# Kernel tuning notes

Measured on AMD Instinct MI355X. Metric: run time of the kernel, lower is better.

The kernel has to match this reference:

```python
import jax, jax.numpy as jnp
import numpy as np

N = 100000        # nodes
E = 1600000       # edges
D = 32            # hidden dim
C = 2             # num classes
NL = 4            # layer_num - 1 GIN layers
G = 512           # graphs in batch
BN_EPS = 1e-3     # keras BatchNormalization default epsilon


def setup_inputs() -> dict:
    key = jax.random.key(0)
    ks = jax.random.split(key, 16)
    s = 0.1
    return {
        "node_embeddings": jax.random.normal(ks[0], (N, D), dtype=jnp.float32),
        "edge_index": jax.random.randint(ks[1], (2, E), 0, N, dtype=jnp.int32),
        "batch": jnp.sort(jax.random.randint(ks[2], (N,), 0, G, dtype=jnp.int32)),
        # MLP inner dense + BN (per GIN layer)
        "W1": jax.random.normal(ks[3], (NL, D, D), dtype=jnp.float32) * s,
        "b1": jnp.zeros((NL, D), jnp.float32),
        "bn1_g": jnp.ones((NL, D), jnp.float32),
        "bn1_b": jnp.zeros((NL, D), jnp.float32),
        # MLP output dense
        "W2": jax.random.normal(ks[4], (NL, D, D), dtype=jnp.float32) * s,
        "b2": jnp.zeros((NL, D), jnp.float32),
        # ApplyNodeFunc BN
        "bn2_g": jnp.ones((NL, D), jnp.float32),
        "bn2_b": jnp.zeros((NL, D), jnp.float32),
        # outer per-layer BN
        "norm_g": jnp.ones((NL, D), jnp.float32),
        "norm_b": jnp.zeros((NL, D), jnp.float32),
        # readout heads: one Dense(num_classes) per hidden_rep level (layer_num of them)
        "dense_W": jax.random.normal(ks[5], (NL + 1, D, C), dtype=jnp.float32) * s,
        "dense_b": jnp.zeros((NL + 1, C), jnp.float32),
    }


def _bn(x, g, b):
    # inference-mode BatchNorm with init moving stats (mean=0, var=1)
    return x * (g / jnp.sqrt(1.0 + BN_EPS)) + b


def reference(node_embeddings, edge_index, batch, W1, b1, bn1_g, bn1_b,
              W2, b2, bn2_g, bn2_b, norm_g, norm_b, dense_W, dense_b):
    src, dst = edge_index[0], edge_index[1]
    h = node_embeddings
    hidden = [h]
    for i in range(NL):
        # GIN aggregation: (1+eps)*h + sum of neighbor features (eps=0)
        agg = jax.ops.segment_sum(h[src], dst, num_segments=N)  # [N, D]
        z = h + agg
        # ApplyNodeFunc: MLP (Dense->BN->ReLU->Dense) then BN + ReLU
        z = jax.nn.relu(_bn(z @ W1[i] + b1[i], bn1_g[i], bn1_b[i]))
        z = z @ W2[i] + b2[i]
        z = jax.nn.relu(_bn(z, bn2_g[i], bn2_b[i]))
        # outer norm + relu
        h = jax.nn.relu(_bn(z, norm_g[i], norm_b[i]))
        hidden.append(h)
    # readout: segment-sum pooling per hidden level, Dense(num_classes), summed
    score = jnp.zeros((G, C), dtype=node_embeddings.dtype)
    for i, hr in enumerate(hidden):
        pool = jax.ops.segment_sum(hr, batch, num_segments=G)  # [G, D]
        score = score + pool @ dense_W[i] + dense_b[i]
    return jax.nn.softmax(score, axis=-1)
```

## Files before the change

### kernel.cpp

```cpp
#include <hip/hip_runtime.h>
#include <hip/hip_fp16.h>

#define NN 100000
#define EE 1600000
#define DD 32
#define CC 2
#define NLAYERS 4
#define GG 512

#define BSH 9
#define BW 512
#define NBUK ((NN + BW - 1) / BW)
#define CAP 12288
#define CH 2048
#define NPART ((EE + CH - 1) / CH)

__global__ void part_kernel(const int* __restrict__ ei,
                            int* __restrict__ gcur,
                            unsigned* __restrict__ part) {
    __shared__ unsigned sorted[CH];
    __shared__ unsigned char sbkt[CH];
    __shared__ int cnt[NBUK], offs[NBUK], cur[NBUK], gbs[NBUK];

    const int tid = threadIdx.x;
    const int eb  = blockIdx.x * CH;
    const int nch = min(CH, EE - eb);

    for (int b = tid; b < NBUK; b += 256) cnt[b] = 0;
    __syncthreads();
    for (int i = tid; i < nch; i += 256) {
        int dn = ei[EE + eb + i];
        atomicAdd(&cnt[dn >> BSH], 1);
    }
    __syncthreads();
    if (tid == 0) {
        int o = 0;
        for (int b = 0; b < NBUK; ++b) { offs[b] = o; o += cnt[b]; }
    }
    __syncthreads();
    if (tid < NBUK) {
        cur[tid] = offs[tid];
        gbs[tid] = cnt[tid] ? atomicAdd(&gcur[tid], cnt[tid]) : 0;
    }
    __syncthreads();
    for (int i = tid; i < nch; i += 256) {
        int s  = ei[eb + i];
        int dn = ei[EE + eb + i];
        int b  = dn >> BSH;
        unsigned pk = ((unsigned)(dn & (BW - 1)) << 17) | (unsigned)s;
        int p = atomicAdd(&cur[b], 1);
        sorted[p] = pk;
        sbkt[p]   = (unsigned char)b;
    }
    __syncthreads();
    for (int i = tid; i < nch; i += 256) {
        int b = sbkt[i];
        part[(size_t)b * CAP + gbs[b] + (i - offs[b])] = sorted[i];
    }
}

__global__ void bscan_kernel(const int* __restrict__ gcur,
                             int* __restrict__ bbase,
                             int* __restrict__ row_ptr) {
    if (threadIdx.x == 0 && blockIdx.x == 0) {
        int o = 0;
        for (int b = 0; b < NBUK; ++b) { bbase[b] = o; o += gcur[b]; }
        row_ptr[NN] = EE;
    }
}

__global__ void lcsr_kernel(const unsigned* __restrict__ part,
                            const int* __restrict__ gcur,
                            const int* __restrict__ bbase,
                            int* __restrict__ row_ptr,
                            int* __restrict__ csr_src) {
    __shared__ int hcnt[BW];
    __shared__ int a[2][BW];
    __shared__ int ccur[BW];
    const int t    = threadIdx.x;
    const int b    = blockIdx.x;
    const int cntb = gcur[b];
    const int base = bbase[b];
    const size_t pb = (size_t)b * CAP;

    hcnt[t] = 0;
    __syncthreads();
    for (int i = t; i < cntb; i += BW)
        atomicAdd(&hcnt[part[pb + i] >> 17], 1);
    __syncthreads();
    int x = hcnt[t];
    a[0][t] = x;
    __syncthreads();
    int cb = 0;
    for (int off = 1; off < BW; off <<= 1) {
        int v = a[cb][t];
        if (t >= off) v += a[cb][t - off];
        a[cb ^ 1][t] = v;
        cb ^= 1;
        __syncthreads();
    }
    const int excl = a[cb][t] - x;
    const int node = b * BW + t;
    if (node < NN) row_ptr[node] = base + excl;
    ccur[t] = excl;
    __syncthreads();
    for (int i = t; i < cntb; i += BW) {
        unsigned pk = part[pb + i];
        int dl  = pk >> 17;
        int pos = base + atomicAdd(&ccur[dl], 1);
        csr_src[pos] = (int)(pk & 0x1FFFFu);
    }
}

__global__ void pool_cvt_kernel(const float* __restrict__ h,
                                const int* __restrict__ batch,
                                const float* __restrict__ Wd,
                                float* __restrict__ score,
                                __half* __restrict__ h16) {
    __shared__ float ss[GG * CC];
    __shared__ float sW[DD * CC];
    const int tid = threadIdx.x;
    for (int i = tid; i < GG * CC; i += 256) ss[i] = 0.f;
    if (tid < DD * CC) sW[tid] = Wd[tid];
    __syncthreads();

    const int d = tid & 31;
    const int grp = tid >> 5;
    const int n0 = blockIdx.x * 512;
    const int n1 = (n0 + 512 < NN) ? (n0 + 512) : NN;

    for (int n = n0 + grp; n < n1; n += 8) {
        float v = h[(size_t)n * DD + d];
        h16[(size_t)n * DD + d] = __float2half_rn(v);
        float p0 = v * sW[d * CC + 0];
        float p1 = v * sW[d * CC + 1];
        #pragma unroll
        for (int off = 16; off > 0; off >>= 1) {
            p0 += __shfl_xor(p0, off, 32);
            p1 += __shfl_xor(p1, off, 32);
        }
        if (d == 0) {
            int g = batch[n];
            atomicAdd(&ss[g * CC + 0], p0);
            atomicAdd(&ss[g * CC + 1], p1);
        }
    }
    __syncthreads();

    for (int i = tid; i < GG * CC; i += 256) {
        float v = ss[i];
        if (v != 0.f) atomicAdd(&score[i], v);
    }
}

__global__ __launch_bounds__(256) void layer_kernel(
    const __half* __restrict__ h_in, __half* __restrict__ h_out,
    const int* __restrict__ row_ptr, const int* __restrict__ csr_src,
    const int* __restrict__ batch,
    const float* __restrict__ W1, const float* __restrict__ b1,
    const float* __restrict__ g1, const float* __restrict__ bt1,
    const float* __restrict__ W2, const float* __restrict__ b2,
    const float* __restrict__ g2, const float* __restrict__ bt2,
    const float* __restrict__ ng, const float* __restrict__ nb,
    const float* __restrict__ dWl, float* __restrict__ score) {
    __shared__ float sp[8 * DD];
    __shared__ float sdW[DD * CC];
    __shared__ float ss[GG * CC];
    __shared__ float zA[64][DD];
    __shared__ float z2loc[8][DD];

    const int tid = threadIdx.x;

    if (tid < DD) {
        sp[0 * DD + tid] = b1[tid];
        sp[1 * DD + tid] = g1[tid];
        sp[2 * DD + tid] = bt1[tid];
        sp[3 * DD + tid] = b2[tid];
        sp[4 * DD + tid] = g2[tid];
        sp[5 * DD + tid] = bt2[tid];
        sp[6 * DD + tid] = ng[tid];
        sp[7 * DD + tid] = nb[tid];
    }
    if (tid < DD * CC) sdW[tid] = dWl[tid];
    for (int i = tid; i < GG * CC; i += 256) ss[i] = 0.f;

    const float invs = 1.0f / sqrtf(1.001f);
    const int base = blockIdx.x * 64;

    {
        const int wav = tid >> 6;
        const int lid = tid & 63;
        const int sub = lid >> 3;
        const int sl  = lid & 7;

        for (int s = 0; s < 16; ++s) {
            const int local = wav * 16 + s;
            const int n = base + local;
            if (n >= NN) break;
            const int e0 = row_ptr[n];
            const int e1 = row_ptr[n + 1];
            float a0 = 0.f, a1 = 0.f, a2 = 0.f, a3 = 0.f;
            for (int t = e0; t < e1; t += 8) {
                const int ee = t + sub;
                const bool ok = ee < e1;
                const int ix = csr_src[ok ? ee : (e1 - 1)];
                const uint2 raw = *reinterpret_cast<const uint2*>(
                    h_in + ((size_t)ix * DD + sl * 4));
                const float2 f01 =
                    __half22float2(*reinterpret_cast<const __half2*>(&raw.x));
                const float2 f23 =
                    __half22float2(*reinterpret_cast<const __half2*>(&raw.y));
                if (ok) { a0 += f01.x; a1 += f01.y; a2 += f23.x; a3 += f23.y; }
            }
            #pragma unroll
            for (int off = 8; off < 64; off <<= 1) {
                a0 += __shfl_xor(a0, off, 64);
                a1 += __shfl_xor(a1, off, 64);
                a2 += __shfl_xor(a2, off, 64);
                a3 += __shfl_xor(a3, off, 64);
            }
            if (lid < 8) {
                const uint2 sraw = *reinterpret_cast<const uint2*>(
                    h_in + ((size_t)n * DD + sl * 4));
                const float2 s01 =
                    __half22float2(*reinterpret_cast<const __half2*>(&sraw.x));
                const float2 s23 =
                    __half22float2(*reinterpret_cast<const __half2*>(&sraw.y));
                float4 r;
                r.x = a0 + s01.x; r.y = a1 + s01.y;
                r.z = a2 + s23.x; r.w = a3 + s23.y;
                *reinterpret_cast<float4*>(&zA[local][sl * 4]) = r;
            }
        }
    }
    __syncthreads();

    const int j = tid >> 5;
    const int d = tid & 31;
    for (int s = 0; s < 8; ++s) {
        const int local = j * 8 + s;
        const int n = base + local;
        if (n >= NN) break;

        float a1 = sp[0 * DD + d];
        #pragma unroll
        for (int kk = 0; kk < DD; kk += 4) {
            const float4 zv = *reinterpret_cast<const float4*>(&zA[local][kk]);
            a1 += zv.x * W1[(kk + 0) * DD + d] + zv.y * W1[(kk + 1) * DD + d] +
                  zv.z * W1[(kk + 2) * DD + d] + zv.w * W1[(kk + 3) * DD + d];
        }
        float v = fmaxf(a1 * (sp[1 * DD + d] * invs) + sp[2 * DD + d], 0.f);
        z2loc[j][d] = v;

        float a2 = sp[3 * DD + d];
        #pragma unroll
        for (int kk = 0; kk < DD; kk += 4) {
            const float4 zv = *reinterpret_cast<const float4*>(&z2loc[j][kk]);
            a2 += zv.x * W2[(kk + 0) * DD + d] + zv.y * W2[(kk + 1) * DD + d] +
                  zv.z * W2[(kk + 2) * DD + d] + zv.w * W2[(kk + 3) * DD + d];
        }
        float w = fmaxf(a2 * (sp[4 * DD + d] * invs) + sp[5 * DD + d], 0.f);
        w = fmaxf(w * (sp[6 * DD + d] * invs) + sp[7 * DD + d], 0.f);
        h_out[(size_t)n * DD + d] = __float2half_rn(w);

        float p0 = w * sdW[d * CC + 0];
        float p1 = w * sdW[d * CC + 1];
        #pragma unroll
        for (int off = 16; off > 0; off >>= 1) {
            p0 += __shfl_xor(p0, off, 32);
            p1 += __shfl_xor(p1, off, 32);
        }
        if (d == 0) {
            int g = batch[n];
            atomicAdd(&ss[g * CC + 0], p0);
            atomicAdd(&ss[g * CC + 1], p1);
        }
    }
    __syncthreads();

    for (int i = tid; i < GG * CC; i += 256) {
        float v = ss[i];
        if (v != 0.f) atomicAdd(&score[i], v);
    }
}

__global__ void softmax_kernel(const float* __restrict__ score,
                               const float* __restrict__ db,
                               float* __restrict__ out) {
    int g = blockIdx.x * blockDim.x + threadIdx.x;
    if (g >= GG) return;
    float bs0 = 0.f, bs1 = 0.f;
    #pragma unroll
    for (int i = 0; i <= NLAYERS; ++i) {
        bs0 += db[i * CC + 0];
        bs1 += db[i * CC + 1];
    }
    float s0 = score[g * CC + 0] + bs0;
    float s1 = score[g * CC + 1] + bs1;
    float m = fmaxf(s0, s1);
    float e0 = expf(s0 - m), e1 = expf(s1 - m);
    float inv = 1.f / (e0 + e1);
    out[g * CC + 0] = e0 * inv;
    out[g * CC + 1] = e1 * inv;
}

extern "C" void kernel_launch(void* const* d_in, const int* in_sizes, int n_in,
                              void* d_out, int out_size, void* d_ws, size_t ws_size,
                              hipStream_t stream) {
    (void)in_sizes; (void)n_in; (void)out_size; (void)ws_size;

    const float* node_emb = (const float*)d_in[0];
    const int*   ei       = (const int*)d_in[1];
    const int*   batch    = (const int*)d_in[2];
    const float* W1       = (const float*)d_in[3];
    const float* b1       = (const float*)d_in[4];
    const float* g1       = (const float*)d_in[5];
    const float* bt1      = (const float*)d_in[6];
    const float* W2       = (const float*)d_in[7];
    const float* b2       = (const float*)d_in[8];
    const float* g2       = (const float*)d_in[9];
    const float* bt2      = (const float*)d_in[10];
    const float* ng       = (const float*)d_in[11];
    const float* nb       = (const float*)d_in[12];
    const float* dW       = (const float*)d_in[13];
    const float* db       = (const float*)d_in[14];
    float* out = (float*)d_out;

    __half* hA16   = (__half*)d_ws;
    __half* hB16   = hA16 + (size_t)NN * DD;
    __half* hC16   = hB16 + (size_t)NN * DD;
    unsigned* part = (unsigned*)hB16;
    float* score   = (float*)(hC16 + (size_t)NN * DD);
    int* row_ptr   = (int*)(score + GG * CC);
    int* csr_src   = row_ptr + NN + 2;
    int* gcur      = csr_src + EE + 16;
    int* bbase     = gcur + 256;

    hipMemsetAsync(gcur, 0, 256 * sizeof(int), stream);
    hipMemsetAsync(score, 0, GG * CC * sizeof(float), stream);

    part_kernel<<<NPART, 256, 0, stream>>>(ei, gcur, part);
    bscan_kernel<<<1, 64, 0, stream>>>(gcur, bbase, row_ptr);
    lcsr_kernel<<<NBUK, BW, 0, stream>>>(part, gcur, bbase, row_ptr, csr_src);

    pool_cvt_kernel<<<(NN + 511) / 512, 256, 0, stream>>>(
        node_emb, batch, dW, score, hC16);

    const int layerGrid = (NN + 63) / 64;
    const __half* cur_in = hC16;
    __half* bufs[2] = {hA16, hB16};
    for (int i = 0; i < NLAYERS; ++i) {
        __half* o = bufs[i & 1];
        layer_kernel<<<layerGrid, 256, 0, stream>>>(
            cur_in, o, row_ptr, csr_src, batch,
            W1 + (size_t)i * DD * DD, b1 + i * DD, g1 + i * DD, bt1 + i * DD,
            W2 + (size_t)i * DD * DD, b2 + i * DD, g2 + i * DD, bt2 + i * DD,
            ng + i * DD, nb + i * DD,
            dW + (size_t)(i + 1) * DD * CC, score);
        cur_in = o;
    }

    softmax_kernel<<<(GG + 255) / 256, 256, 0, stream>>>(score, db, out);
}
```

Baseline: 519.3 us.

## Split neighbor gather by source half to improve L2 locality

The CSR build now partitions each node's edges by whether the source index is in the lower or upper half of the node range, and records a per-node split pointer. Each layer becomes two passes: a new kernel gathers the lower-half sources into an fp32 aggregation buffer, then the layer kernel gathers the upper-half sources and runs the MLP. This keeps each pass's random-gather working set to half the feature table so it fits better in cache. It also switches to one-lane-per-feature gathers with unrolled index batches and nontemporal loads and stores. The cost is an extra launch per layer plus writing and rereading a 100000x32 fp32 buffer.

```diff
diff --git a/kernel.cpp b/kernel.cpp
--- a/kernel.cpp
+++ b/kernel.cpp
@@ -7,6 +7,7 @@
 #define CC 2
 #define NLAYERS 4
 #define GG 512
+#define NHALF 50000
 
 #define BSH 9
 #define BW 512
@@ -14,6 +15,18 @@
 #define CAP 12288
 #define CH 2048
 #define NPART ((EE + CH - 1) / CH)
+
+__device__ __forceinline__ float nt_load_half(const __half* p) {
+    unsigned short u = __builtin_nontemporal_load(
+        reinterpret_cast<const unsigned short*>(p));
+    __half_raw hr; hr.x = u;
+    return __half2float(__half(hr));
+}
+__device__ __forceinline__ void nt_store_half(float v, __half* p) {
+    __half h = __float2half_rn(v);
+    __half_raw hr = *reinterpret_cast<__half_raw*>(&h);
+    __builtin_nontemporal_store(hr.x, reinterpret_cast<unsigned short*>(p));
+}
 
 __global__ void part_kernel(const int* __restrict__ ei,
                             int* __restrict__ gcur,
@@ -73,10 +86,13 @@
                             const int* __restrict__ gcur,
                             const int* __restrict__ bbase,
                             int* __restrict__ row_ptr,
+                            int* __restrict__ row_split,
                             int* __restrict__ csr_src) {
     __shared__ int hcnt[BW];
+    __shared__ int h0cnt[BW];
     __shared__ int a[2][BW];
-    __shared__ int ccur[BW];
+    __shared__ int curA[BW];
+    __shared__ int curB[BW];
     const int t    = threadIdx.x;
     const int b    = blockIdx.x;
     const int cntb = gcur[b];
@@ -84,9 +100,14 @@
     const size_t pb = (size_t)b * CAP;
 
     hcnt[t] = 0;
-    __syncthreads();
-    for (int i = t; i < cntb; i += BW)
-        atomicAdd(&hcnt[part[pb + i] >> 17], 1);
+    h0cnt[t] = 0;
+    __syncthreads();
+    for (int i = t; i < cntb; i += BW) {
+        unsigned pk = part[pb + i];
+        int dl = pk >> 17;
+        atomicAdd(&hcnt[dl], 1);
+        if ((pk & 0x1FFFFu) < NHALF) atomicAdd(&h0cnt[dl], 1);
+    }
     __syncthreads();
     int x = hcnt[t];
     a[0][t] = x;
@@ -101,14 +122,20 @@
     }
     const int excl = a[cb][t] - x;
     const int node = b * BW + t;
-    if (node < NN) row_ptr[node] = base + excl;
-    ccur[t] = excl;
+    if (node < NN) {
+        row_ptr[node]   = base + excl;
+        row_split[node] = base + excl + h0cnt[t];
+    }
+    curA[t] = excl;
+    curB[t] = excl + h0cnt[t];
     __syncthreads();
     for (int i = t; i < cntb; i += BW) {
         unsigned pk = part[pb + i];
         int dl  = pk >> 17;
-        int pos = base + atomicAdd(&ccur[dl], 1);
-        csr_src[pos] = (int)(pk & 0x1FFFFu);
+        int src = (int)(pk & 0x1FFFFu);
+        int pos = base + ((src < NHALF) ? atomicAdd(&curA[dl], 1)
+                                        : atomicAdd(&curB[dl], 1));
+        csr_src[pos] = src;
     }
 }
 
@@ -153,9 +180,79 @@
     }
 }
 
+#define GATHER_LADDER(acc, e, e1)                                             \
+    for (; e + 16 <= e1; e += 16) {                                           \
+        int ix[16];                                                           \
+        _Pragma("unroll")                                                     \
+        for (int i = 0; i < 16; ++i)                                          \
+            ix[i] = __builtin_nontemporal_load(&csr_src[e + i]);              \
+        __half v[16];                                                         \
+        _Pragma("unroll")                                                     \
+        for (int i = 0; i < 16; ++i) v[i] = h_in[(size_t)ix[i] * DD + d];     \
+        float t0 = ((__half2float(v[0]) + __half2float(v[1])) +               \
+                    (__half2float(v[2]) + __half2float(v[3]))) +              \
+                   ((__half2float(v[4]) + __half2float(v[5])) +               \
+                    (__half2float(v[6]) + __half2float(v[7])));               \
+        float t1 = ((__half2float(v[8]) + __half2float(v[9])) +               \
+                    (__half2float(v[10]) + __half2float(v[11]))) +            \
+                   ((__half2float(v[12]) + __half2float(v[13])) +             \
+                    (__half2float(v[14]) + __half2float(v[15])));             \
+        acc += t0 + t1;                                                       \
+    }                                                                         \
+    if (e + 8 <= e1) {                                                        \
+        int ix[8];                                                            \
+        _Pragma("unroll")                                                     \
+        for (int i = 0; i < 8; ++i)                                           \
+            ix[i] = __builtin_nontemporal_load(&csr_src[e + i]);              \
+        __half v[8];                                                          \
+        _Pragma("unroll")                                                     \
+        for (int i = 0; i < 8; ++i) v[i] = h_in[(size_t)ix[i] * DD + d];      \
+        acc += ((__half2float(v[0]) + __half2float(v[1])) +                   \
+                (__half2float(v[2]) + __half2float(v[3]))) +                  \
+               ((__half2float(v[4]) + __half2float(v[5])) +                   \
+                (__half2float(v[6]) + __half2float(v[7])));                   \
+        e += 8;                                                               \
+    }                                                                         \
+    if (e + 4 <= e1) {                                                        \
+        int ix[4];                                                            \
+        _Pragma("unroll")                                                     \
+        for (int i = 0; i < 4; ++i)                                           \
+            ix[i] = __builtin_nontemporal_load(&csr_src[e + i]);              \
+        __half v[4];                                                          \
+        _Pragma("unroll")                                                     \
+        for (int i = 0; i < 4; ++i) v[i] = h_in[(size_t)ix[i] * DD + d];      \
+        acc += (__half2float(v[0]) + __half2float(v[1])) +                    \
+               (__half2float(v[2]) + __half2float(v[3]));                     \
+        e += 4;                                                               \
+    }                                                                         \
+    for (; e < e1; ++e)                                                       \
+        acc += __half2float(h_in[(size_t)csr_src[e] * DD + d]);
+
+__global__ __launch_bounds__(256) void gath0_kernel(
+    const __half* __restrict__ h_in, float* __restrict__ agg,
+    const int* __restrict__ row_ptr, const int* __restrict__ row_split,
+    const int* __restrict__ csr_src) {
+    const int tid = threadIdx.x;
+    const int j = tid >> 5;
+    const int d = tid & 31;
+    const int base = blockIdx.x * 64;
+
+    for (int s = 0; s < 8; ++s) {
+        const int n = base + j * 8 + s;
+        if (n >= NN) break;
+        float acc = nt_load_half(&h_in[(size_t)n * DD + d]);
+        int e = row_ptr[n];
+        const int e1 = row_split[n];
+        GATHER_LADDER(acc, e, e1)
+        __builtin_nontemporal_store(acc, &agg[(size_t)n * DD + d]);
+    }
+}
+
 __global__ __launch_bounds__(256) void layer_kernel(
     const __half* __restrict__ h_in, __half* __restrict__ h_out,
-    const int* __restrict__ row_ptr, const int* __restrict__ csr_src,
+    const float* __restrict__ agg,
+    const int* __restrict__ row_ptr, const int* __restrict__ row_split,
+    const int* __restrict__ csr_src,
     const int* __restrict__ batch,
     const float* __restrict__ W1, const float* __restrict__ b1,
     const float* __restrict__ g1, const float* __restrict__ bt1,
@@ -170,6 +267,8 @@
     __shared__ float z2loc[8][DD];
 
     const int tid = threadIdx.x;
+    const int j = tid >> 5;
+    const int d = tid & 31;
 
     if (tid < DD) {
         sp[0 * DD + tid] = b1[tid];
@@ -187,56 +286,18 @@
     const float invs = 1.0f / sqrtf(1.001f);
     const int base = blockIdx.x * 64;
 
-    {
-        const int wav = tid >> 6;
-        const int lid = tid & 63;
-        const int sub = lid >> 3;
-        const int sl  = lid & 7;
-
-        for (int s = 0; s < 16; ++s) {
-            const int local = wav * 16 + s;
-            const int n = base + local;
-            if (n >= NN) break;
-            const int e0 = row_ptr[n];
-            const int e1 = row_ptr[n + 1];
-            float a0 = 0.f, a1 = 0.f, a2 = 0.f, a3 = 0.f;
-            for (int t = e0; t < e1; t += 8) {
-                const int ee = t + sub;
-                const bool ok = ee < e1;
-                const int ix = csr_src[ok ? ee : (e1 - 1)];
-                const uint2 raw = *reinterpret_cast<const uint2*>(
-                    h_in + ((size_t)ix * DD + sl * 4));
-                const float2 f01 =
-                    __half22float2(*reinterpret_cast<const __half2*>(&raw.x));
-                const float2 f23 =
-                    __half22float2(*reinterpret_cast<const __half2*>(&raw.y));
-                if (ok) { a0 += f01.x; a1 += f01.y; a2 += f23.x; a3 += f23.y; }
-            }
-            #pragma unroll
-            for (int off = 8; off < 64; off <<= 1) {
-                a0 += __shfl_xor(a0, off, 64);
-                a1 += __shfl_xor(a1, off, 64);
-                a2 += __shfl_xor(a2, off, 64);
-                a3 += __shfl_xor(a3, off, 64);
-            }
-            if (lid < 8) {
-                const uint2 sraw = *reinterpret_cast<const uint2*>(
-                    h_in + ((size_t)n * DD + sl * 4));
-                const float2 s01 =
-                    __half22float2(*reinterpret_cast<const __half2*>(&sraw.x));
-                const float2 s23 =
-                    __half22float2(*reinterpret_cast<const __half2*>(&sraw.y));
-                float4 r;
-                r.x = a0 + s01.x; r.y = a1 + s01.y;
-                r.z = a2 + s23.x; r.w = a3 + s23.y;
-                *reinterpret_cast<float4*>(&zA[local][sl * 4]) = r;
-            }
-        }
-    }
-    __syncthreads();
-
-    const int j = tid >> 5;
-    const int d = tid & 31;
+    for (int s = 0; s < 8; ++s) {
+        const int local = j * 8 + s;
+        const int n = base + local;
+        if (n >= NN) break;
+        float acc = __builtin_nontemporal_load(&agg[(size_t)n * DD + d]);
+        int e = row_split[n];
+        const int e1 = row_ptr[n + 1];
+        GATHER_LADDER(acc, e, e1)
+        zA[local][d] = acc;
+    }
+    __syncthreads();
+
     for (int s = 0; s < 8; ++s) {
         const int local = j * 8 + s;
         const int n = base + local;
@@ -261,7 +322,7 @@
         }
         float w = fmaxf(a2 * (sp[4 * DD + d] * invs) + sp[5 * DD + d], 0.f);
         w = fmaxf(w * (sp[6 * DD + d] * invs) + sp[7 * DD + d], 0.f);
-        h_out[(size_t)n * DD + d] = __float2half_rn(w);
+        nt_store_half(w, &h_out[(size_t)n * DD + d]);
 
         float p0 = w * sdW[d * CC + 0];
         float p1 = w * sdW[d * CC + 1];
@@ -335,13 +396,16 @@
     int* csr_src   = row_ptr + NN + 2;
     int* gcur      = csr_src + EE + 16;
     int* bbase     = gcur + 256;
+    int* row_split = bbase + 256;
+    float* agg     = (float*)(row_split + NN);
 
     hipMemsetAsync(gcur, 0, 256 * sizeof(int), stream);
     hipMemsetAsync(score, 0, GG * CC * sizeof(float), stream);
 
     part_kernel<<<NPART, 256, 0, stream>>>(ei, gcur, part);
     bscan_kernel<<<1, 64, 0, stream>>>(gcur, bbase, row_ptr);
-    lcsr_kernel<<<NBUK, BW, 0, stream>>>(part, gcur, bbase, row_ptr, csr_src);
+    lcsr_kernel<<<NBUK, BW, 0, stream>>>(part, gcur, bbase, row_ptr,
+                                         row_split, csr_src);
 
     pool_cvt_kernel<<<(NN + 511) / 512, 256, 0, stream>>>(
         node_emb, batch, dW, score, hC16);
@@ -351,8 +415,10 @@
     __half* bufs[2] = {hA16, hB16};
     for (int i = 0; i < NLAYERS; ++i) {
         __half* o = bufs[i & 1];
+        gath0_kernel<<<layerGrid, 256, 0, stream>>>(
+            cur_in, agg, row_ptr, row_split, csr_src);
         layer_kernel<<<layerGrid, 256, 0, stream>>>(
-            cur_in, o, row_ptr, csr_src, batch,
+            cur_in, o, agg, row_ptr, row_split, csr_src, batch,
             W1 + (size_t)i * DD * DD, b1 + i * DD, g1 + i * DD, bt1 + i * DD,
             W2 + (size_t)i * DD * DD, b2 + i * DD, g2 + i * DD, bt2 + i * DD,
             ng + i * DD, nb + i * DD,
```

New measurement: 567.7 us. 9.3% more time.
